# Performance work log

Hardware: AMD Instinct MI355X
Metric: run time of the kernel (lower is better)

## Reference

```python
import jax, jax.numpy as jnp
import numpy as np

NUM_ITERS = 3
NUM_CAPSULES = 10
NUM_ROUTES = 1152  # 32*6*6
IN_CH = 16
OUT_CH = 32
BATCH = 128


def _squash(t):
    # Faithful to original squash(tensor) with default dim=1 (the batch axis here).
    n2 = jnp.sum(t * t, axis=1, keepdims=True)
    return (n2 / (1.0 + n2)) * t / jnp.sqrt(n2)


def setup_inputs() -> dict:
    key = jax.random.key(0)
    k1, k2 = jax.random.split(key)
    x = jax.random.normal(k1, (BATCH, NUM_ROUTES, IN_CH), dtype=jnp.float32)
    route_weights = jax.random.normal(
        k2, (NUM_CAPSULES, NUM_ROUTES, IN_CH, OUT_CH), dtype=jnp.float32)
    return {"x": x, "route_weights": route_weights}


def reference(x, route_weights):
    # prediction vectors u_hat: [C, B, R, O]
    pred = jnp.einsum('bri,crio->cbro', x, route_weights)
    logits = jnp.zeros_like(pred)  # [C, B, R, O], matching torch zeros of pred size
    outputs = None
    for i in range(NUM_ITERS):
        # routing_softmax with dim=2 -> softmax over the routes axis
        c = jax.nn.softmax(logits, axis=2)
        s = jnp.sum(c * pred, axis=2, keepdims=True)  # [C, B, 1, O]
        outputs = _squash(s)
        if i != NUM_ITERS - 1:
            # delta logits: [C, B, R, 1], broadcasts over O when added
            logits = logits + jnp.sum(pred * outputs, axis=-1, keepdims=True)
    # match torch output shape [C, B, 1, 1, O]
    return outputs[:, :, :, None, :]
```

## Files before the change

### kernel.cpp

```cpp
#include <hip/hip_runtime.h>
#include <math.h>

#define NB 128
#define NR 1152
#define NC 10
#define NCHK 24

typedef __attribute__((ext_vector_type(8))) short bf16x8;
typedef __attribute__((ext_vector_type(16))) float f32x16;

__device__ __forceinline__ unsigned pk_bf16(float a, float b) {
    unsigned r;
    asm("v_cvt_pk_bf16_f32 %0, %1, %2" : "=v"(r) : "v"(a), "v"(b));
    return r;
}

template<int MODE>
__global__ __launch_bounds__(512, 2) void pass_z(const float* __restrict__ x,
                                                 const float* __restrict__ W,
                                                 unsigned* __restrict__ xts,
                                                 float* __restrict__ oacc,
                                                 float* __restrict__ dout,
                                                 float* __restrict__ sbuf,
                                                 float* __restrict__ zbuf,
                                                 int* __restrict__ cnt)
{
    __shared__ float lds[16384];
    __shared__ int lastFlag;
    const int pb = blockIdx.x;
    const int lin = (pb & 7) * 30 + (pb >> 3);
    const int rch = lin / 10;
    const int c   = lin - rch * 10;
    const int t = threadIdx.x;
    const int w = t >> 6, l = t & 63;
    const int h = w >> 1, bp = w & 1;
    const int lo5 = l & 31, hi1 = l >> 5;
    const int r0 = rch * 48 + h * 12;

    if (MODE >= 1) {
        for (int idx = t; idx < 4096; idx += 512)
            lds[(idx >> 5) * 33 + (idx & 31)] = oacc[(size_t)c * 4096 + idx];
    }
    __syncthreads();

    float ov0[16], ov1[16];
    if (MODE >= 1) {
#pragma unroll
        for (int j = 0; j < 16; ++j) {
            int orow = (j & 3) + 8 * (j >> 2) + 4 * hi1;
            ov0[j] = lds[(bp * 64 + lo5) * 33 + orow];
            ov1[j] = lds[(bp * 64 + 32 + lo5) * 33 + orow];
        }
    }

    f32x16 acc0, acc1, zz;
#pragma unroll
    for (int j = 0; j < 16; ++j) { acc0[j] = 0.f; acc1[j] = 0.f; zz[j] = 0.f; }
    float Z0 = 0.f, Z1 = 0.f;

    const float* wb  = W + ((size_t)(c * NR + r0) * 16 + hi1 * 8) * 32 + lo5;
    const float* xp0 = x + ((size_t)(bp * 64 + lo5) * NR + r0) * 16 + hi1 * 8;
    const float* xp1 = x + ((size_t)(bp * 64 + 32 + lo5) * NR + r0) * 16 + hi1 * 8;
    uint4* xt4 = (uint4*)xts;
    const int bq0 = bp * 64 + lo5, bq1 = bq0 + 32;

    for (int rr = 0; rr < 12; ++rr) {
        float wv[8];
#pragma unroll
        for (int j = 0; j < 8; ++j) wv[j] = wb[(size_t)rr * 512 + j * 32];
        union U { uint4 q; unsigned u[4]; bf16x8 v; };
        U Ah, Al, Xh0, Xl0, Xh1, Xl1;
#pragma unroll
        for (int j = 0; j < 4; ++j) Ah.u[j] = pk_bf16(wv[2*j], wv[2*j+1]);
#pragma unroll
        for (int j = 0; j < 4; ++j) {
            float g0 = __uint_as_float(Ah.u[j] << 16);
            float g1 = __uint_as_float(Ah.u[j] & 0xffff0000u);
            Al.u[j] = pk_bf16(wv[2*j] - g0, wv[2*j+1] - g1);
        }
        const size_t rb4 = ((size_t)((r0 + rr) * 2 + hi1) * 2) * 128;
        if (MODE == 0) {
            float4 u0 = *(const float4*)(xp0 + rr * 16);
            float4 u1 = *(const float4*)(xp0 + rr * 16 + 4);
            float4 v0 = *(const float4*)(xp1 + rr * 16);
            float4 v1 = *(const float4*)(xp1 + rr * 16 + 4);
            float xv0[8] = {u0.x,u0.y,u0.z,u0.w, u1.x,u1.y,u1.z,u1.w};
            float xv1[8] = {v0.x,v0.y,v0.z,v0.w, v1.x,v1.y,v1.z,v1.w};
#pragma unroll
            for (int j = 0; j < 4; ++j) Xh0.u[j] = pk_bf16(xv0[2*j], xv0[2*j+1]);
#pragma unroll
            for (int j = 0; j < 4; ++j) {
                float g0 = __uint_as_float(Xh0.u[j] << 16);
                float g1 = __uint_as_float(Xh0.u[j] & 0xffff0000u);
                Xl0.u[j] = pk_bf16(xv0[2*j] - g0, xv0[2*j+1] - g1);
            }
#pragma unroll
            for (int j = 0; j < 4; ++j) Xh1.u[j] = pk_bf16(xv1[2*j], xv1[2*j+1]);
#pragma unroll
            for (int j = 0; j < 4; ++j) {
                float g0 = __uint_as_float(Xh1.u[j] << 16);
                float g1 = __uint_as_float(Xh1.u[j] & 0xffff0000u);
                Xl1.u[j] = pk_bf16(xv1[2*j] - g0, xv1[2*j+1] - g1);
            }
            if (((h * 12 + rr) % 10) == c) {
                xt4[rb4 + bq0]       = Xh0.q;
                xt4[rb4 + 128 + bq0] = Xl0.q;
                xt4[rb4 + bq1]       = Xh1.q;
                xt4[rb4 + 128 + bq1] = Xl1.q;
            }
        } else {
            Xh0.q = xt4[rb4 + bq0];
            Xl0.q = xt4[rb4 + 128 + bq0];
            Xh1.q = xt4[rb4 + bq1];
            Xl1.q = xt4[rb4 + 128 + bq1];
        }

        if (MODE == 0) {
            acc0 = __builtin_amdgcn_mfma_f32_32x32x16_bf16(Ah.v, Xh0.v, acc0, 0, 0, 0);
            acc0 = __builtin_amdgcn_mfma_f32_32x32x16_bf16(Al.v, Xh0.v, acc0, 0, 0, 0);
            acc0 = __builtin_amdgcn_mfma_f32_32x32x16_bf16(Ah.v, Xl0.v, acc0, 0, 0, 0);
            acc1 = __builtin_amdgcn_mfma_f32_32x32x16_bf16(Ah.v, Xh1.v, acc1, 0, 0, 0);
            acc1 = __builtin_amdgcn_mfma_f32_32x32x16_bf16(Al.v, Xh1.v, acc1, 0, 0, 0);
            acc1 = __builtin_amdgcn_mfma_f32_32x32x16_bf16(Ah.v, Xl1.v, acc1, 0, 0, 0);
        } else {
            f32x16 q0, q1;
            q0 = __builtin_amdgcn_mfma_f32_32x32x16_bf16(Ah.v, Xh0.v, zz, 0, 0, 0);
            q1 = __builtin_amdgcn_mfma_f32_32x32x16_bf16(Ah.v, Xh1.v, zz, 0, 0, 0);
            q0 = __builtin_amdgcn_mfma_f32_32x32x16_bf16(Al.v, Xh0.v, q0, 0, 0, 0);
            q1 = __builtin_amdgcn_mfma_f32_32x32x16_bf16(Al.v, Xh1.v, q1, 0, 0, 0);
            q0 = __builtin_amdgcn_mfma_f32_32x32x16_bf16(Ah.v, Xl0.v, q0, 0, 0, 0);
            q1 = __builtin_amdgcn_mfma_f32_32x32x16_bf16(Ah.v, Xl1.v, q1, 0, 0, 0);
            float d0 = 0.f, d1 = 0.f;
#pragma unroll
            for (int j = 0; j < 16; ++j) {
                d0 = fmaf(q0[j], ov0[j], d0);
                d1 = fmaf(q1[j], ov1[j], d1);
            }
            d0 += __shfl_xor(d0, 32);
            d1 += __shfl_xor(d1, 32);
            float e0 = __expf(d0 - 20.0f);
            float e1 = __expf(d1 - 20.0f);
            Z0 += e0; Z1 += e1;
#pragma unroll
            for (int j = 0; j < 16; ++j) {
                acc0[j] = fmaf(e0, q0[j], acc0[j]);
                acc1[j] = fmaf(e1, q1[j], acc1[j]);
            }
        }
    }

    const int b0 = bp * 64 + lo5, b1 = b0 + 32;
    __syncthreads();
#pragma unroll
    for (int j = 0; j < 16; ++j) {
        int orow = (j & 3) + 8 * (j >> 2) + 4 * hi1;
        lds[h * 4096 + b0 * 32 + (orow ^ lo5)] = acc0[j];
        lds[h * 4096 + b1 * 32 + (orow ^ lo5)] = acc1[j];
    }
    __syncthreads();
    float* sc = sbuf + (size_t)c * 4096;
    for (int idx = t; idx < 4096; idx += 512) {
        int b = idx >> 5, o = idx & 31;
        float s = 0.f;
#pragma unroll
        for (int hh = 0; hh < 4; ++hh)
            s += lds[hh * 4096 + b * 32 + (o ^ (b & 31))];
        (void)__hip_atomic_fetch_add(sc + idx, s, __ATOMIC_RELAXED,
                                     __HIP_MEMORY_SCOPE_AGENT);
    }
    if (MODE >= 1) {
        __syncthreads();
        if (l < 32) {
            lds[h * 128 + bp * 64 + lo5] = Z0;
            lds[h * 128 + bp * 64 + 32 + lo5] = Z1;
        }
        __syncthreads();
        if (t < 128) {
            float z = lds[t] + lds[128 + t] + lds[256 + t] + lds[384 + t];
            (void)__hip_atomic_fetch_add(zbuf + (size_t)c * 128 + t, z,
                                         __ATOMIC_RELAXED, __HIP_MEMORY_SCOPE_AGENT);
        }
    }

    __syncthreads();
    if (t == 0) {
        int old = __hip_atomic_fetch_add(&cnt[c], 1,
                                         __ATOMIC_RELAXED, __HIP_MEMORY_SCOPE_AGENT);
        lastFlag = (old == NCHK - 1) ? 1 : 0;
    }
    __syncthreads();
    if (!lastFlag) return;

    if (MODE >= 1) {
        if (t < NB) {
            lds[8192 + t] = __hip_atomic_load(zbuf + (size_t)c * 128 + t,
                                              __ATOMIC_RELAXED, __HIP_MEMORY_SCOPE_AGENT);
        }
        __syncthreads();
    }
    float sv[8];
    float pn = 0.f;
#pragma unroll
    for (int k = 0; k < 8; ++k) {
        int idx = t + 512 * k;
        float s = __hip_atomic_load(sc + idx, __ATOMIC_RELAXED,
                                    __HIP_MEMORY_SCOPE_AGENT);
        float v = (MODE == 0) ? s * (1.0f / 1152.0f) : s / lds[8192 + (idx >> 5)];
        sv[k] = v;
        pn = fmaf(v, v, pn);
    }
    lds[(t >> 5) * 33 + (t & 31)] = pn;
    __syncthreads();
    if (t < 32) {
        float n2 = 0.f;
#pragma unroll
        for (int m = 0; m < 16; ++m) n2 += lds[m * 33 + t];
        lds[1024 + t] = sqrtf(n2) / (1.0f + n2);
    }
    __syncthreads();
    const float ff = lds[1024 + (t & 31)];
#pragma unroll
    for (int k = 0; k < 8; ++k) {
        int idx = t + 512 * k;
        float v = sv[k] * ff;
        if (MODE == 0)      oacc[(size_t)c * 4096 + idx] = v;
        else if (MODE == 1) oacc[(size_t)c * 4096 + idx] += v;
        else                dout[(size_t)c * 4096 + idx] = v;
    }
}

extern "C" void kernel_launch(void* const* d_in, const int* in_sizes, int n_in,
                              void* d_out, int out_size, void* d_ws, size_t ws_size,
                              hipStream_t stream)
{
    (void)in_sizes; (void)n_in; (void)out_size; (void)ws_size;
    const float* x = (const float*)d_in[0];
    const float* W = (const float*)d_in[1];
    float* wsf  = (float*)d_ws;
    float* outf = (float*)d_out;

    unsigned* xts = (unsigned*)d_ws;
    float* sb   = wsf + 2359296;
    float* zb   = sb + 3 * 40960;
    int*   cnt  = (int*)(zb + 3 * 1280);
    float* oacc = (float*)(cnt + 32);

    hipMemsetAsync(sb, 0, (size_t)(3 * 40960 + 3 * 1280 + 32) * 4, stream);

    pass_z<0><<<240, 512, 0, stream>>>(x, W, xts, oacc, nullptr,
                                       sb, zb, cnt);
    pass_z<1><<<240, 512, 0, stream>>>(x, W, xts, oacc, nullptr,
                                       sb + 40960, zb + 1280, cnt + NC);
    pass_z<2><<<240, 512, 0, stream>>>(x, W, xts, oacc, outf,
                                       sb + 2 * 40960, zb + 2 * 1280, cnt + 2 * NC);
}
```

Before: 67.74 us.

## Fuse routing iterations 1 and 2 into one kernel with a grid-wide spin barrier

Replaces three launches with two: pass 0 only accumulates partial sums, and a fused kernel performs iterations 1 and 2. Every block recomputes the squash from the global sums itself, so the separate last-block merge step and the oacc buffer are gone. Blocks wait on per-capsule atomic counters between the iterations, which removes a kernel launch and a tail-block serialization. The spin wait relies on all 240 blocks being co-resident, which the launch bounds of 2 blocks per CU allow on this GPU, and it adds redundant squash work in every block.

```diff
diff --git a/kernel.cpp b/kernel.cpp
--- a/kernel.cpp
+++ b/kernel.cpp
@@ -16,52 +16,24 @@
 }
 
 template<int MODE>
-__global__ __launch_bounds__(512, 2) void pass_z(const float* __restrict__ x,
-                                                 const float* __restrict__ W,
-                                                 unsigned* __restrict__ xts,
-                                                 float* __restrict__ oacc,
-                                                 float* __restrict__ dout,
-                                                 float* __restrict__ sbuf,
-                                                 float* __restrict__ zbuf,
-                                                 int* __restrict__ cnt)
-{
-    __shared__ float lds[16384];
-    __shared__ int lastFlag;
-    const int pb = blockIdx.x;
-    const int lin = (pb & 7) * 30 + (pb >> 3);
-    const int rch = lin / 10;
-    const int c   = lin - rch * 10;
-    const int t = threadIdx.x;
-    const int w = t >> 6, l = t & 63;
-    const int h = w >> 1, bp = w & 1;
-    const int lo5 = l & 31, hi1 = l >> 5;
-    const int r0 = rch * 48 + h * 12;
-
-    if (MODE >= 1) {
-        for (int idx = t; idx < 4096; idx += 512)
-            lds[(idx >> 5) * 33 + (idx & 31)] = oacc[(size_t)c * 4096 + idx];
-    }
-    __syncthreads();
-
-    float ov0[16], ov1[16];
-    if (MODE >= 1) {
-#pragma unroll
-        for (int j = 0; j < 16; ++j) {
-            int orow = (j & 3) + 8 * (j >> 2) + 4 * hi1;
-            ov0[j] = lds[(bp * 64 + lo5) * 33 + orow];
-            ov1[j] = lds[(bp * 64 + 32 + lo5) * 33 + orow];
-        }
-    }
-
-    f32x16 acc0, acc1, zz;
+__device__ __forceinline__ void route_mainloop(
+    const float* __restrict__ x, const float* __restrict__ W,
+    uint4* __restrict__ xt4,
+    int c, int r0, int bp, int lo5, int hi1,
+    const float (&ov0)[16], const float (&ov1)[16],
+    f32x16& acc0, f32x16& acc1, float& Z0, float& Z1)
+{
+    f32x16 zz;
 #pragma unroll
     for (int j = 0; j < 16; ++j) { acc0[j] = 0.f; acc1[j] = 0.f; zz[j] = 0.f; }
-    float Z0 = 0.f, Z1 = 0.f;
-
-    const float* wb  = W + ((size_t)(c * NR + r0) * 16 + hi1 * 8) * 32 + lo5;
-    const float* xp0 = x + ((size_t)(bp * 64 + lo5) * NR + r0) * 16 + hi1 * 8;
-    const float* xp1 = x + ((size_t)(bp * 64 + 32 + lo5) * NR + r0) * 16 + hi1 * 8;
-    uint4* xt4 = (uint4*)xts;
+    Z0 = 0.f; Z1 = 0.f;
+
+    const float* wb = W + ((size_t)(c * NR + r0) * 16 + hi1 * 8) * 32 + lo5;
+    const float* xp0 = nullptr, * xp1 = nullptr;
+    if (MODE == 0) {
+        xp0 = x + ((size_t)(bp * 64 + lo5) * NR + r0) * 16 + hi1 * 8;
+        xp1 = x + ((size_t)(bp * 64 + 32 + lo5) * NR + r0) * 16 + hi1 * 8;
+    }
     const int bq0 = bp * 64 + lo5, bq1 = bq0 + 32;
 
     for (int rr = 0; rr < 12; ++rr) {
@@ -102,7 +74,7 @@
                 float g1 = __uint_as_float(Xh1.u[j] & 0xffff0000u);
                 Xl1.u[j] = pk_bf16(xv1[2*j] - g0, xv1[2*j+1] - g1);
             }
-            if (((h * 12 + rr) % 10) == c) {
+            if ((((r0 + rr) % 48) % 10) == c) {
                 xt4[rb4 + bq0]       = Xh0.q;
                 xt4[rb4 + 128 + bq0] = Xl0.q;
                 xt4[rb4 + bq1]       = Xh1.q;
@@ -148,7 +120,14 @@
             }
         }
     }
-
+}
+
+template<int WITHZ>
+__device__ __forceinline__ void chunk_atomic_add(
+    const f32x16& acc0, const f32x16& acc1, float Z0, float Z1,
+    int t, int l, int h, int bp, int lo5, int hi1,
+    float* lds, float* __restrict__ sc, float* __restrict__ zc)
+{
     const int b0 = bp * 64 + lo5, b1 = b0 + 32;
     __syncthreads();
 #pragma unroll
@@ -158,7 +137,6 @@
         lds[h * 4096 + b1 * 32 + (orow ^ lo5)] = acc1[j];
     }
     __syncthreads();
-    float* sc = sbuf + (size_t)c * 4096;
     for (int idx = t; idx < 4096; idx += 512) {
         int b = idx >> 5, o = idx & 31;
         float s = 0.f;
@@ -168,7 +146,7 @@
         (void)__hip_atomic_fetch_add(sc + idx, s, __ATOMIC_RELAXED,
                                      __HIP_MEMORY_SCOPE_AGENT);
     }
-    if (MODE >= 1) {
+    if (WITHZ) {
         __syncthreads();
         if (l < 32) {
             lds[h * 128 + bp * 64 + lo5] = Z0;
@@ -177,56 +155,149 @@
         __syncthreads();
         if (t < 128) {
             float z = lds[t] + lds[128 + t] + lds[256 + t] + lds[384 + t];
-            (void)__hip_atomic_fetch_add(zbuf + (size_t)c * 128 + t, z,
-                                         __ATOMIC_RELAXED, __HIP_MEMORY_SCOPE_AGENT);
-        }
-    }
-
-    __syncthreads();
-    if (t == 0) {
-        int old = __hip_atomic_fetch_add(&cnt[c], 1,
-                                         __ATOMIC_RELAXED, __HIP_MEMORY_SCOPE_AGENT);
-        lastFlag = (old == NCHK - 1) ? 1 : 0;
-    }
-    __syncthreads();
-    if (!lastFlag) return;
-
-    if (MODE >= 1) {
-        if (t < NB) {
-            lds[8192 + t] = __hip_atomic_load(zbuf + (size_t)c * 128 + t,
-                                              __ATOMIC_RELAXED, __HIP_MEMORY_SCOPE_AGENT);
-        }
-        __syncthreads();
-    }
-    float sv[8];
+            (void)__hip_atomic_fetch_add(zc + t, z, __ATOMIC_RELAXED,
+                                         __HIP_MEMORY_SCOPE_AGENT);
+        }
+    }
+}
+
+template<int M, bool ATOM>
+__device__ __forceinline__ void merge_squash(
+    const float* __restrict__ sc, const float* __restrict__ zc,
+    int t, float* lds, float (&sv)[8])
+{
+    if (M >= 1 && t < NB) {
+        float z = ATOM ? __hip_atomic_load(zc + t, __ATOMIC_RELAXED,
+                                           __HIP_MEMORY_SCOPE_AGENT)
+                       : zc[t];
+        lds[5120 + t] = z;
+    }
+    __syncthreads();
     float pn = 0.f;
 #pragma unroll
     for (int k = 0; k < 8; ++k) {
         int idx = t + 512 * k;
-        float s = __hip_atomic_load(sc + idx, __ATOMIC_RELAXED,
-                                    __HIP_MEMORY_SCOPE_AGENT);
-        float v = (MODE == 0) ? s * (1.0f / 1152.0f) : s / lds[8192 + (idx >> 5)];
+        float s = ATOM ? __hip_atomic_load(sc + idx, __ATOMIC_RELAXED,
+                                           __HIP_MEMORY_SCOPE_AGENT)
+                       : sc[idx];
+        float v = (M == 0) ? s * (1.0f / 1152.0f) : s / lds[5120 + (idx >> 5)];
         sv[k] = v;
         pn = fmaf(v, v, pn);
-    }
-    lds[(t >> 5) * 33 + (t & 31)] = pn;
+        lds[(idx >> 5) * 33 + (idx & 31)] = v;
+    }
+    lds[4480 + (t >> 5) * 33 + (t & 31)] = pn;
     __syncthreads();
     if (t < 32) {
         float n2 = 0.f;
 #pragma unroll
-        for (int m = 0; m < 16; ++m) n2 += lds[m * 33 + t];
-        lds[1024 + t] = sqrtf(n2) / (1.0f + n2);
-    }
-    __syncthreads();
-    const float ff = lds[1024 + (t & 31)];
-#pragma unroll
-    for (int k = 0; k < 8; ++k) {
-        int idx = t + 512 * k;
-        float v = sv[k] * ff;
-        if (MODE == 0)      oacc[(size_t)c * 4096 + idx] = v;
-        else if (MODE == 1) oacc[(size_t)c * 4096 + idx] += v;
-        else                dout[(size_t)c * 4096 + idx] = v;
-    }
+        for (int m = 0; m < 16; ++m) n2 += lds[4480 + m * 33 + t];
+        lds[5008 + t] = sqrtf(n2) / (1.0f + n2);
+    }
+    __syncthreads();
+}
+
+__global__ __launch_bounds__(512, 2) void pass0_k(const float* __restrict__ x,
+                                                  const float* __restrict__ W,
+                                                  unsigned* __restrict__ xts,
+                                                  float* __restrict__ sb)
+{
+    __shared__ float lds[16384];
+    const int pb = blockIdx.x;
+    const int lin = (pb & 7) * 30 + (pb >> 3);
+    const int rch = lin / 10;
+    const int c   = lin - rch * 10;
+    const int t = threadIdx.x;
+    const int w = t >> 6, l = t & 63;
+    const int h = w >> 1, bp = w & 1;
+    const int lo5 = l & 31, hi1 = l >> 5;
+    const int r0 = rch * 48 + h * 12;
+
+    float dum0[16], dum1[16];
+    f32x16 acc0, acc1; float Z0, Z1;
+    route_mainloop<0>(x, W, (uint4*)xts, c, r0, bp, lo5, hi1,
+                      dum0, dum1, acc0, acc1, Z0, Z1);
+    chunk_atomic_add<0>(acc0, acc1, Z0, Z1, t, l, h, bp, lo5, hi1,
+                        lds, sb + (size_t)c * 4096, nullptr);
+}
+
+__global__ __launch_bounds__(512, 2) void fused12_k(const float* __restrict__ W,
+                                                    unsigned* __restrict__ xts,
+                                                    float* __restrict__ dout,
+                                                    float* __restrict__ sb,
+                                                    float* __restrict__ zb,
+                                                    int* __restrict__ cnt)
+{
+    __shared__ float lds[16384];
+    const int pb = blockIdx.x;
+    const int lin = (pb & 7) * 30 + (pb >> 3);
+    const int rch = lin / 10;
+    const int c   = lin - rch * 10;
+    const int t = threadIdx.x;
+    const int w = t >> 6, l = t & 63;
+    const int h = w >> 1, bp = w & 1;
+    const int lo5 = l & 31, hi1 = l >> 5;
+    const int r0 = rch * 48 + h * 12;
+    uint4* xt4 = (uint4*)xts;
+
+    float ov0[16], ov1[16], sv[8];
+
+    merge_squash<0, false>(sb + (size_t)c * 4096, nullptr, t, lds, sv);
+#pragma unroll
+    for (int j = 0; j < 16; ++j) {
+        int orow = (j & 3) + 8 * (j >> 2) + 4 * hi1;
+        float ffj = lds[5008 + orow];
+        ov0[j] = lds[(bp * 64 + lo5) * 33 + orow] * ffj;
+        ov1[j] = lds[(bp * 64 + 32 + lo5) * 33 + orow] * ffj;
+    }
+
+    f32x16 acc0, acc1; float Z0, Z1;
+    route_mainloop<1>(nullptr, W, xt4, c, r0, bp, lo5, hi1,
+                      ov0, ov1, acc0, acc1, Z0, Z1);
+    float* sc1 = sb + (size_t)(NC + c) * 4096;
+    float* zc1 = zb + (size_t)c * 128;
+    chunk_atomic_add<1>(acc0, acc1, Z0, Z1, t, l, h, bp, lo5, hi1, lds, sc1, zc1);
+
+    __syncthreads();
+    if (t == 0) {
+        __hip_atomic_fetch_add(&cnt[c], 1, __ATOMIC_RELAXED, __HIP_MEMORY_SCOPE_AGENT);
+        while (__hip_atomic_load(&cnt[c], __ATOMIC_RELAXED,
+                                 __HIP_MEMORY_SCOPE_AGENT) < NCHK)
+            __builtin_amdgcn_s_sleep(4);
+    }
+    __syncthreads();
+
+    merge_squash<1, true>(sc1, zc1, t, lds, sv);
+#pragma unroll
+    for (int j = 0; j < 16; ++j) {
+        int orow = (j & 3) + 8 * (j >> 2) + 4 * hi1;
+        float ffj = lds[5008 + orow];
+        ov0[j] += lds[(bp * 64 + lo5) * 33 + orow] * ffj;
+        ov1[j] += lds[(bp * 64 + 32 + lo5) * 33 + orow] * ffj;
+    }
+
+    route_mainloop<1>(nullptr, W, xt4, c, r0, bp, lo5, hi1,
+                      ov0, ov1, acc0, acc1, Z0, Z1);
+    float* sc2 = sb + (size_t)(2 * NC + c) * 4096;
+    float* zc2 = zb + (size_t)(NC + c) * 128;
+    chunk_atomic_add<1>(acc0, acc1, Z0, Z1, t, l, h, bp, lo5, hi1, lds, sc2, zc2);
+
+    __syncthreads();
+    if (t == 0)
+        __hip_atomic_fetch_add(&cnt[NC + c], 1, __ATOMIC_RELAXED,
+                               __HIP_MEMORY_SCOPE_AGENT);
+    if (rch != 0) return;
+    if (t == 0) {
+        while (__hip_atomic_load(&cnt[NC + c], __ATOMIC_RELAXED,
+                                 __HIP_MEMORY_SCOPE_AGENT) < NCHK)
+            __builtin_amdgcn_s_sleep(4);
+    }
+    __syncthreads();
+
+    merge_squash<2, true>(sc2, zc2, t, lds, sv);
+    const float ff2 = lds[5008 + (t & 31)];
+#pragma unroll
+    for (int k = 0; k < 8; ++k)
+        dout[(size_t)c * 4096 + t + 512 * k] = sv[k] * ff2;
 }
 
 extern "C" void kernel_launch(void* const* d_in, const int* in_sizes, int n_in,
@@ -240,17 +311,12 @@
     float* outf = (float*)d_out;
 
     unsigned* xts = (unsigned*)d_ws;
-    float* sb   = wsf + 2359296;
-    float* zb   = sb + 3 * 40960;
-    int*   cnt  = (int*)(zb + 3 * 1280);
-    float* oacc = (float*)(cnt + 32);
-
-    hipMemsetAsync(sb, 0, (size_t)(3 * 40960 + 3 * 1280 + 32) * 4, stream);
-
-    pass_z<0><<<240, 512, 0, stream>>>(x, W, xts, oacc, nullptr,
-                                       sb, zb, cnt);
-    pass_z<1><<<240, 512, 0, stream>>>(x, W, xts, oacc, nullptr,
-                                       sb + 40960, zb + 1280, cnt + NC);
-    pass_z<2><<<240, 512, 0, stream>>>(x, W, xts, oacc, outf,
-                                       sb + 2 * 40960, zb + 2 * 1280, cnt + 2 * NC);
-}
+    float* sb  = wsf + 2359296;
+    float* zb  = sb + 3 * 40960;
+    int*   cnt = (int*)(zb + 2 * 1280);
+
+    hipMemsetAsync(sb, 0, (size_t)(3 * 40960 + 2 * 1280 + 32) * 4, stream);
+
+    pass0_k<<<240, 512, 0, stream>>>(x, W, xts, sb);
+    fused12_k<<<240, 512, 0, stream>>>(W, xts, outf, sb, zb, cnt);
+}
```

New measurement: 68.07 us. About the same (+0.5%).

## Fuse three routing passes into one persistent kernel with grid barriers

Applied to the files above, without the earlier changes.

Replaces the three per-iteration kernel launches with a single kernel of 480 blocks that synchronises through atomic counters and spin-waits between routing iterations. Each block now handles half of the batch, which doubles parallelism and halves per-thread accumulators. Routing outputs are kept in registers across iterations instead of going through a global accumulator buffer. This removes launch gaps and global round trips, but relies on all blocks being co-resident and adds spin-barrier latency plus redundant W loads per batch half.

```diff
diff --git a/kernel.cpp b/kernel.cpp
--- a/kernel.cpp
+++ b/kernel.cpp
@@ -4,7 +4,8 @@
 #define NB 128
 #define NR 1152
 #define NC 10
-#define NCHK 24
+#define NBLK 480
+#define NPC  48
 
 typedef __attribute__((ext_vector_type(8))) short bf16x8;
 typedef __attribute__((ext_vector_type(16))) float f32x16;
@@ -15,61 +16,30 @@
     return r;
 }
 
+union UF { uint4 q; unsigned u[4]; bf16x8 v; };
+
 template<int MODE>
-__global__ __launch_bounds__(512, 2) void pass_z(const float* __restrict__ x,
-                                                 const float* __restrict__ W,
-                                                 unsigned* __restrict__ xts,
-                                                 float* __restrict__ oacc,
-                                                 float* __restrict__ dout,
-                                                 float* __restrict__ sbuf,
-                                                 float* __restrict__ zbuf,
-                                                 int* __restrict__ cnt)
-{
-    __shared__ float lds[16384];
-    __shared__ int lastFlag;
-    const int pb = blockIdx.x;
-    const int lin = (pb & 7) * 30 + (pb >> 3);
-    const int rch = lin / 10;
-    const int c   = lin - rch * 10;
-    const int t = threadIdx.x;
-    const int w = t >> 6, l = t & 63;
-    const int h = w >> 1, bp = w & 1;
-    const int lo5 = l & 31, hi1 = l >> 5;
-    const int r0 = rch * 48 + h * 12;
-
-    if (MODE >= 1) {
-        for (int idx = t; idx < 4096; idx += 512)
-            lds[(idx >> 5) * 33 + (idx & 31)] = oacc[(size_t)c * 4096 + idx];
-    }
-    __syncthreads();
-
-    float ov0[16], ov1[16];
-    if (MODE >= 1) {
-#pragma unroll
-        for (int j = 0; j < 16; ++j) {
-            int orow = (j & 3) + 8 * (j >> 2) + 4 * hi1;
-            ov0[j] = lds[(bp * 64 + lo5) * 33 + orow];
-            ov1[j] = lds[(bp * 64 + 32 + lo5) * 33 + orow];
-        }
-    }
-
-    f32x16 acc0, acc1, zz;
-#pragma unroll
-    for (int j = 0; j < 16; ++j) { acc0[j] = 0.f; acc1[j] = 0.f; zz[j] = 0.f; }
-    float Z0 = 0.f, Z1 = 0.f;
-
-    const float* wb  = W + ((size_t)(c * NR + r0) * 16 + hi1 * 8) * 32 + lo5;
-    const float* xp0 = x + ((size_t)(bp * 64 + lo5) * NR + r0) * 16 + hi1 * 8;
-    const float* xp1 = x + ((size_t)(bp * 64 + 32 + lo5) * NR + r0) * 16 + hi1 * 8;
-    uint4* xt4 = (uint4*)xts;
-    const int bq0 = bp * 64 + lo5, bq1 = bq0 + 32;
-
+__device__ __forceinline__ void mainloop(const float* __restrict__ x,
+                                         const float* __restrict__ W,
+                                         uint4* __restrict__ xt4,
+                                         int c, int r0, int bq, int lo5, int hi1,
+                                         int lr0,
+                                         const float (&ov)[16],
+                                         f32x16& acc, float& Z)
+{
+    f32x16 zz;
+#pragma unroll
+    for (int j = 0; j < 16; ++j) { acc[j] = 0.f; zz[j] = 0.f; }
+    Z = 0.f;
+    const float* wb = W + ((size_t)(c * NR + r0) * 16 + hi1 * 8) * 32 + lo5;
+    const float* xp = (MODE == 0) ? x + ((size_t)bq * NR + r0) * 16 + hi1 * 8 : nullptr;
+
+#pragma unroll 3
     for (int rr = 0; rr < 12; ++rr) {
         float wv[8];
 #pragma unroll
         for (int j = 0; j < 8; ++j) wv[j] = wb[(size_t)rr * 512 + j * 32];
-        union U { uint4 q; unsigned u[4]; bf16x8 v; };
-        U Ah, Al, Xh0, Xl0, Xh1, Xl1;
+        UF Ah, Al, Xh, Xl;
 #pragma unroll
         for (int j = 0; j < 4; ++j) Ah.u[j] = pk_bf16(wv[2*j], wv[2*j+1]);
 #pragma unroll
@@ -80,153 +50,199 @@
         }
         const size_t rb4 = ((size_t)((r0 + rr) * 2 + hi1) * 2) * 128;
         if (MODE == 0) {
-            float4 u0 = *(const float4*)(xp0 + rr * 16);
-            float4 u1 = *(const float4*)(xp0 + rr * 16 + 4);
-            float4 v0 = *(const float4*)(xp1 + rr * 16);
-            float4 v1 = *(const float4*)(xp1 + rr * 16 + 4);
-            float xv0[8] = {u0.x,u0.y,u0.z,u0.w, u1.x,u1.y,u1.z,u1.w};
-            float xv1[8] = {v0.x,v0.y,v0.z,v0.w, v1.x,v1.y,v1.z,v1.w};
-#pragma unroll
-            for (int j = 0; j < 4; ++j) Xh0.u[j] = pk_bf16(xv0[2*j], xv0[2*j+1]);
+            float4 u0 = *(const float4*)(xp + rr * 16);
+            float4 u1 = *(const float4*)(xp + rr * 16 + 4);
+            float xv[8] = {u0.x,u0.y,u0.z,u0.w, u1.x,u1.y,u1.z,u1.w};
+#pragma unroll
+            for (int j = 0; j < 4; ++j) Xh.u[j] = pk_bf16(xv[2*j], xv[2*j+1]);
 #pragma unroll
             for (int j = 0; j < 4; ++j) {
-                float g0 = __uint_as_float(Xh0.u[j] << 16);
-                float g1 = __uint_as_float(Xh0.u[j] & 0xffff0000u);
-                Xl0.u[j] = pk_bf16(xv0[2*j] - g0, xv0[2*j+1] - g1);
+                float g0 = __uint_as_float(Xh.u[j] << 16);
+                float g1 = __uint_as_float(Xh.u[j] & 0xffff0000u);
+                Xl.u[j] = pk_bf16(xv[2*j] - g0, xv[2*j+1] - g1);
             }
-#pragma unroll
-            for (int j = 0; j < 4; ++j) Xh1.u[j] = pk_bf16(xv1[2*j], xv1[2*j+1]);
-#pragma unroll
-            for (int j = 0; j < 4; ++j) {
-                float g0 = __uint_as_float(Xh1.u[j] << 16);
-                float g1 = __uint_as_float(Xh1.u[j] & 0xffff0000u);
-                Xl1.u[j] = pk_bf16(xv1[2*j] - g0, xv1[2*j+1] - g1);
+            if (((lr0 + rr) % 10) == c) {
+                xt4[rb4 + bq]       = Xh.q;
+                xt4[rb4 + 128 + bq] = Xl.q;
             }
-            if (((h * 12 + rr) % 10) == c) {
-                xt4[rb4 + bq0]       = Xh0.q;
-                xt4[rb4 + 128 + bq0] = Xl0.q;
-                xt4[rb4 + bq1]       = Xh1.q;
-                xt4[rb4 + 128 + bq1] = Xl1.q;
+            acc = __builtin_amdgcn_mfma_f32_32x32x16_bf16(Ah.v, Xh.v, acc, 0, 0, 0);
+            acc = __builtin_amdgcn_mfma_f32_32x32x16_bf16(Al.v, Xh.v, acc, 0, 0, 0);
+            acc = __builtin_amdgcn_mfma_f32_32x32x16_bf16(Ah.v, Xl.v, acc, 0, 0, 0);
+        } else {
+            Xh.q = xt4[rb4 + bq];
+            Xl.q = xt4[rb4 + 128 + bq];
+            f32x16 q;
+            q = __builtin_amdgcn_mfma_f32_32x32x16_bf16(Ah.v, Xh.v, zz, 0, 0, 0);
+            q = __builtin_amdgcn_mfma_f32_32x32x16_bf16(Al.v, Xh.v, q, 0, 0, 0);
+            q = __builtin_amdgcn_mfma_f32_32x32x16_bf16(Ah.v, Xl.v, q, 0, 0, 0);
+            float d0 = 0.f, d1 = 0.f;
+#pragma unroll
+            for (int j = 0; j < 8; ++j) {
+                d0 = fmaf(q[2*j],   ov[2*j],   d0);
+                d1 = fmaf(q[2*j+1], ov[2*j+1], d1);
             }
-        } else {
-            Xh0.q = xt4[rb4 + bq0];
-            Xl0.q = xt4[rb4 + 128 + bq0];
-            Xh1.q = xt4[rb4 + bq1];
-            Xl1.q = xt4[rb4 + 128 + bq1];
+            float d = d0 + d1;
+            d += __shfl_xor(d, 32);
+            float e = __expf(d - 20.0f);
+            Z += e;
+#pragma unroll
+            for (int j = 0; j < 16; ++j) acc[j] = fmaf(e, q[j], acc[j]);
         }
-
-        if (MODE == 0) {
-            acc0 = __builtin_amdgcn_mfma_f32_32x32x16_bf16(Ah.v, Xh0.v, acc0, 0, 0, 0);
-            acc0 = __builtin_amdgcn_mfma_f32_32x32x16_bf16(Al.v, Xh0.v, acc0, 0, 0, 0);
-            acc0 = __builtin_amdgcn_mfma_f32_32x32x16_bf16(Ah.v, Xl0.v, acc0, 0, 0, 0);
-            acc1 = __builtin_amdgcn_mfma_f32_32x32x16_bf16(Ah.v, Xh1.v, acc1, 0, 0, 0);
-            acc1 = __builtin_amdgcn_mfma_f32_32x32x16_bf16(Al.v, Xh1.v, acc1, 0, 0, 0);
-            acc1 = __builtin_amdgcn_mfma_f32_32x32x16_bf16(Ah.v, Xl1.v, acc1, 0, 0, 0);
-        } else {
-            f32x16 q0, q1;
-            q0 = __builtin_amdgcn_mfma_f32_32x32x16_bf16(Ah.v, Xh0.v, zz, 0, 0, 0);
-            q1 = __builtin_amdgcn_mfma_f32_32x32x16_bf16(Ah.v, Xh1.v, zz, 0, 0, 0);
-            q0 = __builtin_amdgcn_mfma_f32_32x32x16_bf16(Al.v, Xh0.v, q0, 0, 0, 0);
-            q1 = __builtin_amdgcn_mfma_f32_32x32x16_bf16(Al.v, Xh1.v, q1, 0, 0, 0);
-            q0 = __builtin_amdgcn_mfma_f32_32x32x16_bf16(Ah.v, Xl0.v, q0, 0, 0, 0);
-            q1 = __builtin_amdgcn_mfma_f32_32x32x16_bf16(Ah.v, Xl1.v, q1, 0, 0, 0);
-            float d0 = 0.f, d1 = 0.f;
-#pragma unroll
-            for (int j = 0; j < 16; ++j) {
-                d0 = fmaf(q0[j], ov0[j], d0);
-                d1 = fmaf(q1[j], ov1[j], d1);
-            }
-            d0 += __shfl_xor(d0, 32);
-            d1 += __shfl_xor(d1, 32);
-            float e0 = __expf(d0 - 20.0f);
-            float e1 = __expf(d1 - 20.0f);
-            Z0 += e0; Z1 += e1;
-#pragma unroll
-            for (int j = 0; j < 16; ++j) {
-                acc0[j] = fmaf(e0, q0[j], acc0[j]);
-                acc1[j] = fmaf(e1, q1[j], acc1[j]);
-            }
-        }
-    }
-
-    const int b0 = bp * 64 + lo5, b1 = b0 + 32;
+    }
+}
+
+template<int WITHZ>
+__device__ __forceinline__ void chunk_add(const f32x16& acc, float Z,
+    int t, int l, int h, int bp, int bh, int lo5, int hi1,
+    float* lds, float* __restrict__ sc, float* __restrict__ zc)
+{
+    const int bl = bp * 32 + lo5;
     __syncthreads();
 #pragma unroll
     for (int j = 0; j < 16; ++j) {
         int orow = (j & 3) + 8 * (j >> 2) + 4 * hi1;
-        lds[h * 4096 + b0 * 32 + (orow ^ lo5)] = acc0[j];
-        lds[h * 4096 + b1 * 32 + (orow ^ lo5)] = acc1[j];
-    }
-    __syncthreads();
-    float* sc = sbuf + (size_t)c * 4096;
-    for (int idx = t; idx < 4096; idx += 512) {
-        int b = idx >> 5, o = idx & 31;
+        lds[h * 2048 + bl * 32 + (orow ^ lo5)] = acc[j];
+    }
+    __syncthreads();
+#pragma unroll
+    for (int k = 0; k < 4; ++k) {
+        int idx = t + 512 * k;
+        int b2 = idx >> 5, o = idx & 31;
         float s = 0.f;
 #pragma unroll
         for (int hh = 0; hh < 4; ++hh)
-            s += lds[hh * 4096 + b * 32 + (o ^ (b & 31))];
-        (void)__hip_atomic_fetch_add(sc + idx, s, __ATOMIC_RELAXED,
-                                     __HIP_MEMORY_SCOPE_AGENT);
-    }
-    if (MODE >= 1) {
+            s += lds[hh * 2048 + b2 * 32 + (o ^ (b2 & 31))];
+        (void)__hip_atomic_fetch_add(sc + (size_t)(bh * 64 + b2) * 32 + o, s,
+                                     __ATOMIC_RELAXED, __HIP_MEMORY_SCOPE_AGENT);
+    }
+    if (WITHZ) {
         __syncthreads();
-        if (l < 32) {
-            lds[h * 128 + bp * 64 + lo5] = Z0;
-            lds[h * 128 + bp * 64 + 32 + lo5] = Z1;
-        }
+        if (l < 32) lds[8192 + h * 64 + bp * 32 + l] = Z;
         __syncthreads();
-        if (t < 128) {
-            float z = lds[t] + lds[128 + t] + lds[256 + t] + lds[384 + t];
-            (void)__hip_atomic_fetch_add(zbuf + (size_t)c * 128 + t, z,
+        if (t < 64) {
+            float z = lds[8192 + t] + lds[8256 + t] + lds[8320 + t] + lds[8384 + t];
+            (void)__hip_atomic_fetch_add(zc + bh * 64 + t, z,
                                          __ATOMIC_RELAXED, __HIP_MEMORY_SCOPE_AGENT);
         }
     }
-
-    __syncthreads();
-    if (t == 0) {
-        int old = __hip_atomic_fetch_add(&cnt[c], 1,
-                                         __ATOMIC_RELAXED, __HIP_MEMORY_SCOPE_AGENT);
-        lastFlag = (old == NCHK - 1) ? 1 : 0;
-    }
-    __syncthreads();
-    if (!lastFlag) return;
-
-    if (MODE >= 1) {
-        if (t < NB) {
-            lds[8192 + t] = __hip_atomic_load(zbuf + (size_t)c * 128 + t,
-                                              __ATOMIC_RELAXED, __HIP_MEMORY_SCOPE_AGENT);
-        }
-        __syncthreads();
-    }
-    float sv[8];
+}
+
+template<int M>
+__device__ __forceinline__ void merge_squash(const float* __restrict__ sc,
+                                             const float* __restrict__ zc,
+                                             int t, float* lds, float (&sv)[8])
+{
+    if (M >= 1 && t < NB)
+        lds[5120 + t] = __hip_atomic_load(zc + t, __ATOMIC_RELAXED,
+                                          __HIP_MEMORY_SCOPE_AGENT);
+    __syncthreads();
     float pn = 0.f;
 #pragma unroll
     for (int k = 0; k < 8; ++k) {
         int idx = t + 512 * k;
         float s = __hip_atomic_load(sc + idx, __ATOMIC_RELAXED,
                                     __HIP_MEMORY_SCOPE_AGENT);
-        float v = (MODE == 0) ? s * (1.0f / 1152.0f) : s / lds[8192 + (idx >> 5)];
+        float v = (M == 0) ? s * (1.0f / 1152.0f) : s / lds[5120 + (idx >> 5)];
         sv[k] = v;
         pn = fmaf(v, v, pn);
-    }
-    lds[(t >> 5) * 33 + (t & 31)] = pn;
+        lds[(idx >> 5) * 33 + (idx & 31)] = v;
+    }
+    lds[4480 + (t >> 5) * 33 + (t & 31)] = pn;
     __syncthreads();
     if (t < 32) {
         float n2 = 0.f;
 #pragma unroll
-        for (int m = 0; m < 16; ++m) n2 += lds[m * 33 + t];
-        lds[1024 + t] = sqrtf(n2) / (1.0f + n2);
-    }
-    __syncthreads();
-    const float ff = lds[1024 + (t & 31)];
-#pragma unroll
-    for (int k = 0; k < 8; ++k) {
-        int idx = t + 512 * k;
-        float v = sv[k] * ff;
-        if (MODE == 0)      oacc[(size_t)c * 4096 + idx] = v;
-        else if (MODE == 1) oacc[(size_t)c * 4096 + idx] += v;
-        else                dout[(size_t)c * 4096 + idx] = v;
-    }
+        for (int m = 0; m < 16; ++m) n2 += lds[4480 + m * 33 + t];
+        lds[5008 + t] = sqrtf(n2) / (1.0f + n2);
+    }
+    __syncthreads();
+}
+
+__global__ __launch_bounds__(512, 4) void routing_k(const float* __restrict__ x,
+                                                    const float* __restrict__ W,
+                                                    unsigned* __restrict__ xts,
+                                                    float* __restrict__ dout,
+                                                    float* __restrict__ sb,
+                                                    float* __restrict__ zb,
+                                                    int* __restrict__ cnt)
+{
+    __shared__ float lds[16384];
+    const int pb = blockIdx.x;
+    const int lin = (pb & 7) * 60 + (pb >> 3);
+    const int c   = lin % 10;
+    const int qq  = lin / 10;
+    const int bh  = qq & 1;
+    const int rch = qq >> 1;
+    const int t = threadIdx.x;
+    const int w = t >> 6, l = t & 63;
+    const int h = w >> 1, bp = w & 1;
+    const int lo5 = l & 31, hi1 = l >> 5;
+    const int r0 = rch * 48 + h * 12;
+    const int bq = bh * 64 + bp * 32 + lo5;
+    uint4* xt4 = (uint4*)xts;
+
+    float ov[16], sv[8];
+    f32x16 acc; float Z;
+#pragma unroll
+    for (int j = 0; j < 16; ++j) ov[j] = 0.f;
+
+    mainloop<0>(x, W, xt4, c, r0, bq, lo5, hi1, h * 12, ov, acc, Z);
+    chunk_add<0>(acc, Z, t, l, h, bp, bh, lo5, hi1, lds,
+                 sb + (size_t)c * 4096, nullptr);
+    __syncthreads();
+    if (t == 0) {
+        __hip_atomic_fetch_add(&cnt[0], 1, __ATOMIC_RELAXED, __HIP_MEMORY_SCOPE_AGENT);
+        while (__hip_atomic_load(&cnt[0], __ATOMIC_RELAXED,
+                                 __HIP_MEMORY_SCOPE_AGENT) < NBLK)
+            __builtin_amdgcn_s_sleep(8);
+    }
+    __syncthreads();
+    merge_squash<0>(sb + (size_t)c * 4096, nullptr, t, lds, sv);
+#pragma unroll
+    for (int j = 0; j < 16; ++j) {
+        int orow = (j & 3) + 8 * (j >> 2) + 4 * hi1;
+        ov[j] = lds[bq * 33 + orow] * lds[5008 + orow];
+    }
+
+    float* sc1 = sb + (size_t)(NC + c) * 4096;
+    float* zc1 = zb + (size_t)c * 128;
+    mainloop<1>(nullptr, W, xt4, c, r0, bq, lo5, hi1, 0, ov, acc, Z);
+    chunk_add<1>(acc, Z, t, l, h, bp, bh, lo5, hi1, lds, sc1, zc1);
+    __syncthreads();
+    if (t == 0) {
+        __hip_atomic_fetch_add(&cnt[1 + c], 1, __ATOMIC_RELAXED, __HIP_MEMORY_SCOPE_AGENT);
+        while (__hip_atomic_load(&cnt[1 + c], __ATOMIC_RELAXED,
+                                 __HIP_MEMORY_SCOPE_AGENT) < NPC)
+            __builtin_amdgcn_s_sleep(8);
+    }
+    __syncthreads();
+    merge_squash<1>(sc1, zc1, t, lds, sv);
+#pragma unroll
+    for (int j = 0; j < 16; ++j) {
+        int orow = (j & 3) + 8 * (j >> 2) + 4 * hi1;
+        ov[j] += lds[bq * 33 + orow] * lds[5008 + orow];
+    }
+
+    float* sc2 = sb + (size_t)(2 * NC + c) * 4096;
+    float* zc2 = zb + (size_t)(NC + c) * 128;
+    mainloop<1>(nullptr, W, xt4, c, r0, bq, lo5, hi1, 0, ov, acc, Z);
+    chunk_add<1>(acc, Z, t, l, h, bp, bh, lo5, hi1, lds, sc2, zc2);
+    __syncthreads();
+    if (t == 0)
+        __hip_atomic_fetch_add(&cnt[11 + c], 1, __ATOMIC_RELAXED,
+                               __HIP_MEMORY_SCOPE_AGENT);
+    if (rch != 0 || bh != 0) return;
+    if (t == 0) {
+        while (__hip_atomic_load(&cnt[11 + c], __ATOMIC_RELAXED,
+                                 __HIP_MEMORY_SCOPE_AGENT) < NPC)
+            __builtin_amdgcn_s_sleep(8);
+    }
+    __syncthreads();
+    merge_squash<2>(sc2, zc2, t, lds, sv);
+    const float ff = lds[5008 + (t & 31)];
+#pragma unroll
+    for (int k = 0; k < 8; ++k)
+        dout[(size_t)c * 4096 + t + 512 * k] = sv[k] * ff;
 }
 
 extern "C" void kernel_launch(void* const* d_in, const int* in_sizes, int n_in,
@@ -240,17 +256,11 @@
     float* outf = (float*)d_out;
 
     unsigned* xts = (unsigned*)d_ws;
-    float* sb   = wsf + 2359296;
-    float* zb   = sb + 3 * 40960;
-    int*   cnt  = (int*)(zb + 3 * 1280);
-    float* oacc = (float*)(cnt + 32);
-
-    hipMemsetAsync(sb, 0, (size_t)(3 * 40960 + 3 * 1280 + 32) * 4, stream);
-
-    pass_z<0><<<240, 512, 0, stream>>>(x, W, xts, oacc, nullptr,
-                                       sb, zb, cnt);
-    pass_z<1><<<240, 512, 0, stream>>>(x, W, xts, oacc, nullptr,
-                                       sb + 40960, zb + 1280, cnt + NC);
-    pass_z<2><<<240, 512, 0, stream>>>(x, W, xts, oacc, outf,
-                                       sb + 2 * 40960, zb + 2 * 1280, cnt + 2 * NC);
-}
+    float* sb  = wsf + 2359296;
+    float* zb  = sb + 3 * NC * 4096;
+    int*   cnt = (int*)(zb + 2 * NC * 128);
+
+    hipMemsetAsync(sb, 0, (size_t)(3 * NC * 4096 + 2 * NC * 128 + 64) * 4, stream);
+
+    routing_k<<<NBLK, 512, 0, stream>>>(x, W, xts, outf, sb, zb, cnt);
+}
```

After: 117.7 us. +73.8%, slower.
